# Kernel tuning notes

Measured on AMD Instinct MI355X. Metric: run time of the kernel, lower is better.

## Reference

```python
import jax, jax.numpy as jnp
import numpy as np

B, L, H = 32, 2048, 1024


def setup_inputs() -> dict:
    key = jax.random.key(0)
    k1, k2, k3, k4, k5 = jax.random.split(key, 5)
    stdv = 1.0 / np.sqrt(H)
    return {
        "hidden": jax.random.normal(k1, (B, H), dtype=jnp.float32),
        "encoder_outputs": jax.random.normal(k2, (L, B, H), dtype=jnp.float32),
        "attn_w": jax.random.normal(k3, (H, 2 * H), dtype=jnp.float32) * stdv,
        "attn_b": jax.random.normal(k4, (H,), dtype=jnp.float32) * stdv,
        "v": jax.random.normal(k5, (H,), dtype=jnp.float32) * stdv,
    }


def reference(hidden, encoder_outputs, attn_w, attn_b, v):
    # encoder_outputs: [L, B, H] -> batch-first [B, L, H]
    enc = jnp.transpose(encoder_outputs, (1, 0, 2))
    # Additive (Bahdanau) energies. Split the concat-linear into two GEMMs to
    # avoid materializing the [B, L, 2H] concat:
    #   attn([H_rep, enc]) = hidden @ W_h^T + enc @ W_e^T + b
    w_h, w_e = attn_w[:, :H], attn_w[:, H:]  # each [H, 2H]->[H, H]
    proj = (jnp.einsum("bh,oh->bo", hidden, w_h)[:, None, :]
            + jnp.einsum("blh,oh->blo", enc, w_e)
            + attn_b)
    energy = jnp.tanh(proj)                   # [B, L, H]
    scores = jnp.einsum("blh,h->bl", energy, v)  # [B, L]
    attn = jax.nn.softmax(scores, axis=-1)       # [B, L]
    context = jnp.einsum("bl,blh->bh", attn, enc)  # [B, H]
    return context[None, :, :]  # [1, B, H] matching context.transpose(0,1)
```

## Files before the change

### kernel.cpp

```cpp
#include <hip/hip_runtime.h>
#include <hip/hip_bf16.h>
#include <math.h>

#define Hdim 1024
#define Bdim 32
#define Ldim 2048
#define Mtot (Bdim*Ldim)

typedef __attribute__((ext_vector_type(8))) short short8v;
typedef __attribute__((ext_vector_type(4))) short short4v;
typedef __attribute__((ext_vector_type(4))) float floatx4;

static __device__ inline short f2bf(float f) {
    union { float f; unsigned u; } x; x.f = f;
    unsigned r = x.u + 0x7FFF + ((x.u >> 16) & 1);
    return (short)(r >> 16);
}
static __device__ inline float bf2f(short s) {
    union { unsigned u; float f; } x; x.u = ((unsigned)(unsigned short)s) << 16;
    return x.f;
}

static __device__ inline float fast_tanh(float x) {
    float t = 2.0f * x;
    t = fminf(fmaxf(t, -30.0f), 30.0f);
    float e = __expf(t);
    return (e - 1.0f) / (e + 1.0f);
}

typedef __attribute__((address_space(1))) const void GVT;
typedef __attribute__((address_space(3))) void LVT;
static __device__ inline void gload_lds16(const void* g, void* l) {
    __builtin_amdgcn_global_load_lds((GVT*)g, (LVT*)l, 16, 0, 0);
}

__global__ __launch_bounds__(256) void convert_enc_kernel(
    const float* __restrict__ enc, short* __restrict__ enc_bf)
{
    size_t i = ((size_t)blockIdx.x * 256 + threadIdx.x) * 8;
    float4 a = *(const float4*)(enc + i);
    float4 b = *(const float4*)(enc + i + 4);
    short8v o;
    o[0]=f2bf(a.x); o[1]=f2bf(a.y); o[2]=f2bf(a.z); o[3]=f2bf(a.w);
    o[4]=f2bf(b.x); o[5]=f2bf(b.y); o[6]=f2bf(b.z); o[7]=f2bf(b.w);
    *(short8v*)(enc_bf + i) = o;
}

__global__ __launch_bounds__(256) void convert_w_kernel(
    const float* __restrict__ attn_w, short* __restrict__ w_bf)
{
    int t = blockIdx.x * 256 + threadIdx.x;
    int o = t >> 7;
    int c = t & 127;
    const float* src = attn_w + (size_t)o * 2 * Hdim + Hdim + c * 8;
    float4 a = *(const float4*)(src);
    float4 b = *(const float4*)(src + 4);
    short8v v;
    v[0]=f2bf(a.x); v[1]=f2bf(a.y); v[2]=f2bf(a.z); v[3]=f2bf(a.w);
    v[4]=f2bf(b.x); v[5]=f2bf(b.y); v[6]=f2bf(b.z); v[7]=f2bf(b.w);
    *(short8v*)(w_bf + (size_t)o * Hdim + c * 8) = v;
}

__global__ __launch_bounds__(256) void qproj_kernel(
    const float* __restrict__ hidden, const float* __restrict__ attn_w,
    const float* __restrict__ attn_b, float* __restrict__ qbuf)
{
    int w = blockIdx.x * 4 + (threadIdx.x >> 6);
    int lane = threadIdx.x & 63;
    int o = w >> 5;
    int b = w & 31;
    const float* hrow = hidden + b * Hdim;
    const float* wrow = attn_w + (size_t)o * 2 * Hdim;
    float s = 0.f;
    #pragma unroll
    for (int i = 0; i < 16; i++) s += hrow[lane + i*64] * wrow[lane + i*64];
    s += __shfl_xor(s, 1);  s += __shfl_xor(s, 2);  s += __shfl_xor(s, 4);
    s += __shfl_xor(s, 8);  s += __shfl_xor(s, 16); s += __shfl_xor(s, 32);
    if (lane == 0) qbuf[b * Hdim + o] = s + attn_b[o];
}

#define BM 128
#define BN 128
#define BK 32

__global__ __launch_bounds__(256, 4) void scores_kernel(
    const short* __restrict__ enc_bf,
    const short* __restrict__ w_bf,
    const float* __restrict__ qbuf,
    const float* __restrict__ vvec,
    float* __restrict__ spart)
{
    __shared__ short As[2][BM * BK];
    __shared__ short Bs[2][BN * BK];
    __shared__ float sred[BM][2];

    int hw = blockIdx.x;
    int xcd = hw & 7;
    int i5  = hw >> 3;
    int nblk  = i5 & 7;
    int mtile = xcd * 64 + (i5 >> 3);
    int m0 = mtile * BM;
    int n0 = nblk * BN;

    int tid  = threadIdx.x;
    int w    = tid >> 6;
    int l    = tid & 63;
    int wr = w >> 1, wc = w & 1;
    int r15 = l & 15;
    int kc  = l >> 4;

    int subrow = l >> 2;
    int chunk  = l & 3;
    const short* ag0 = enc_bf + (size_t)(m0 + w*32 + subrow) * Hdim + chunk * 8;
    const short* ag1 = ag0 + (size_t)16 * Hdim;
    const short* bg0 = w_bf  + (size_t)(n0 + w*32 + subrow) * Hdim + chunk * 8;
    const short* bg1 = bg0 + (size_t)16 * Hdim;
    int al0 = (w*32) * BK;
    int al1 = (w*32 + 16) * BK;

    int aoff[4], boff[4];
    #pragma unroll
    for (int i = 0; i < 4; i++) {
        aoff[i] = (wr*64 + i*16 + r15) * BK + kc * 8;
        boff[i] = (wc*64 + i*16 + r15) * BK + kc * 8;
    }

    floatx4 acc[4][4];
    #pragma unroll
    for (int i = 0; i < 4; i++)
        #pragma unroll
        for (int j = 0; j < 4; j++) acc[i][j] = (floatx4){0.f, 0.f, 0.f, 0.f};

    gload_lds16(ag0, &As[0][al0]);
    gload_lds16(ag1, &As[0][al1]);
    gload_lds16(bg0, &Bs[0][al0]);
    gload_lds16(bg1, &Bs[0][al1]);
    ag0 += BK; ag1 += BK; bg0 += BK; bg1 += BK;
    __syncthreads();

    #pragma unroll 2
    for (int kt = 0; kt < Hdim / BK; kt++) {
        int cur = kt & 1;
        if (kt < Hdim / BK - 1) {
            int nxt = cur ^ 1;
            gload_lds16(ag0, &As[nxt][al0]);
            gload_lds16(ag1, &As[nxt][al1]);
            gload_lds16(bg0, &Bs[nxt][al0]);
            gload_lds16(bg1, &Bs[nxt][al1]);
            ag0 += BK; ag1 += BK; bg0 += BK; bg1 += BK;
        }
        short8v af[4], bf[4];
        #pragma unroll
        for (int mi = 0; mi < 4; mi++) af[mi] = *(const short8v*)(&As[cur][aoff[mi]]);
        #pragma unroll
        for (int ni = 0; ni < 4; ni++) bf[ni] = *(const short8v*)(&Bs[cur][boff[ni]]);
        #pragma unroll
        for (int mi = 0; mi < 4; mi++)
            #pragma unroll
            for (int ni = 0; ni < 4; ni++)
                acc[mi][ni] = __builtin_amdgcn_mfma_f32_16x16x32_bf16(af[mi], bf[ni], acc[mi][ni], 0, 0, 0);
        __syncthreads();
    }

    int rg = l >> 4;
    #pragma unroll
    for (int mi = 0; mi < 4; mi++) {
        float rs[4] = {0.f, 0.f, 0.f, 0.f};
        #pragma unroll
        for (int ni = 0; ni < 4; ni++) {
            int o = n0 + wc*64 + ni*16 + r15;
            float vo = vvec[o];
            #pragma unroll
            for (int reg = 0; reg < 4; reg++) {
                int trow = wr*64 + mi*16 + rg*4 + reg;
                int b = trow & 31;
                float p = acc[mi][ni][reg] + qbuf[b * Hdim + o];
                rs[reg] += fast_tanh(p) * vo;
            }
        }
        #pragma unroll
        for (int reg = 0; reg < 4; reg++) {
            float s = rs[reg];
            s += __shfl_xor(s, 1); s += __shfl_xor(s, 2);
            s += __shfl_xor(s, 4); s += __shfl_xor(s, 8);
            if (r15 == 0) {
                int trow = wr*64 + mi*16 + rg*4 + reg;
                sred[trow][wc] = s;
            }
        }
    }
    __syncthreads();
    if (tid < BM)
        spart[(size_t)nblk * Mtot + m0 + tid] = sred[tid][0] + sred[tid][1];
}

__global__ __launch_bounds__(256) void softmax_kernel(
    const float* __restrict__ spart, float* __restrict__ attn)
{
    int b = blockIdx.x;
    int t = threadIdx.x;
    __shared__ float rmax[4], rsum[4];
    float sv[8];
    float mx = -1e30f;
    #pragma unroll
    for (int i = 0; i < 8; i++) {
        int l = t + i * 256;
        int m = l * Bdim + b;
        float s = 0.f;
        #pragma unroll
        for (int p = 0; p < 8; p++) s += spart[(size_t)p * Mtot + m];
        sv[i] = s;
        mx = fmaxf(mx, s);
    }
    #pragma unroll
    for (int off = 1; off < 64; off <<= 1) mx = fmaxf(mx, __shfl_xor(mx, off));
    if ((t & 63) == 0) rmax[t >> 6] = mx;
    __syncthreads();
    mx = fmaxf(fmaxf(rmax[0], rmax[1]), fmaxf(rmax[2], rmax[3]));
    float sum = 0.f;
    #pragma unroll
    for (int i = 0; i < 8; i++) { sv[i] = __expf(sv[i] - mx); sum += sv[i]; }
    #pragma unroll
    for (int off = 1; off < 64; off <<= 1) sum += __shfl_xor(sum, off);
    if ((t & 63) == 0) rsum[t >> 6] = sum;
    __syncthreads();
    sum = rsum[0] + rsum[1] + rsum[2] + rsum[3];
    float inv = 1.f / sum;
    #pragma unroll
    for (int i = 0; i < 8; i++)
        attn[(size_t)b * Ldim + t + i * 256] = sv[i] * inv;
}

__global__ __launch_bounds__(256) void context_part_kernel(
    const short* __restrict__ enc_bf,
    const float* __restrict__ attn,
    float* __restrict__ cpart)
{
    int b = blockIdx.x & 31;
    int c = blockIdx.x >> 5;
    int t = threadIdx.x;
    float a0 = 0.f, a1 = 0.f, a2 = 0.f, a3 = 0.f;
    int l0 = c * 32;
    for (int i = 0; i < 32; i++) {
        int l = l0 + i;
        float a = attn[(size_t)b * Ldim + l];
        short4v e = *(const short4v*)(enc_bf + (size_t)(l * Bdim + b) * Hdim + t * 4);
        a0 += a * bf2f(e.x); a1 += a * bf2f(e.y);
        a2 += a * bf2f(e.z); a3 += a * bf2f(e.w);
    }
    float4 r; r.x = a0; r.y = a1; r.z = a2; r.w = a3;
    *(float4*)(cpart + ((size_t)c * Bdim + b) * Hdim + t * 4) = r;
}

__global__ __launch_bounds__(256) void context_reduce_kernel(
    const float* __restrict__ cpart, float* __restrict__ out)
{
    int idx = blockIdx.x * 256 + threadIdx.x;
    float s = 0.f;
    for (int c = 0; c < 64; c++) s += cpart[(size_t)c * (Bdim * Hdim) + idx];
    out[idx] = s;
}

extern "C" void kernel_launch(void* const* d_in, const int* in_sizes, int n_in,
                              void* d_out, int out_size, void* d_ws, size_t ws_size,
                              hipStream_t stream)
{
    const float* hidden = (const float*)d_in[0];
    const float* enc    = (const float*)d_in[1];
    const float* attn_w = (const float*)d_in[2];
    const float* attn_b = (const float*)d_in[3];
    const float* vvec   = (const float*)d_in[4];
    float* out = (float*)d_out;

    char* ws = (char*)d_ws;
    size_t off = 0;
    short* enc_bf = (short*)(ws + off); off += (size_t)Mtot * Hdim * 2;
    short* w_bf   = (short*)(ws + off); off += (size_t)Hdim * Hdim * 2;
    float* qbuf   = (float*)(ws + off); off += (size_t)Bdim * Hdim * 4;
    float* spart  = (float*)(ws + off); off += (size_t)8 * Mtot * 4;
    float* attnp  = (float*)(ws + off); off += (size_t)Mtot * 4;
    float* cpart  = (float*)(ws + off);

    convert_enc_kernel<<<32768, 256, 0, stream>>>(enc, enc_bf);
    convert_w_kernel<<<512, 256, 0, stream>>>(attn_w, w_bf);
    qproj_kernel<<<8192, 256, 0, stream>>>(hidden, attn_w, attn_b, qbuf);
    scores_kernel<<<4096, 256, 0, stream>>>(enc_bf, w_bf, qbuf, vvec, spart);
    softmax_kernel<<<Bdim, 256, 0, stream>>>(spart, attnp);
    context_part_kernel<<<2048, 256, 0, stream>>>(enc_bf, attnp, cpart);
    context_reduce_kernel<<<128, 256, 0, stream>>>(cpart, out);
}
```

Measured before the change: 306.7 us.

## Fuse encoder bf16 conversion into scores GEMM A-tile load and drop convert pass

Removes the separate kernel that converted the whole encoder tensor to bf16. The scores GEMM now loads fp32 encoder rows into registers, converts them, and writes them into XOR-swizzled LDS, with the conversion of the next tile overlapped with the current MFMA work. The B tile also uses a matching swizzle, and the context kernel now reads fp32 encoder directly. This avoids a full write-then-reread of a 128MB-class intermediate. In exchange, the GEMM reads fp32 A once per N-block (8 times), doubling its A-side bytes, and it uses more registers.

```diff
diff --git a/kernel.cpp b/kernel.cpp
--- a/kernel.cpp
+++ b/kernel.cpp
@@ -16,9 +16,9 @@
     unsigned r = x.u + 0x7FFF + ((x.u >> 16) & 1);
     return (short)(r >> 16);
 }
-static __device__ inline float bf2f(short s) {
-    union { unsigned u; float f; } x; x.u = ((unsigned)(unsigned short)s) << 16;
-    return x.f;
+static __device__ inline short f2bf_hw(float f) {
+    __hip_bfloat16 h = __float2bfloat16(f);
+    return *reinterpret_cast<short*>(&h);
 }
 
 static __device__ inline float fast_tanh(float x) {
@@ -32,18 +32,6 @@
 typedef __attribute__((address_space(3))) void LVT;
 static __device__ inline void gload_lds16(const void* g, void* l) {
     __builtin_amdgcn_global_load_lds((GVT*)g, (LVT*)l, 16, 0, 0);
-}
-
-__global__ __launch_bounds__(256) void convert_enc_kernel(
-    const float* __restrict__ enc, short* __restrict__ enc_bf)
-{
-    size_t i = ((size_t)blockIdx.x * 256 + threadIdx.x) * 8;
-    float4 a = *(const float4*)(enc + i);
-    float4 b = *(const float4*)(enc + i + 4);
-    short8v o;
-    o[0]=f2bf(a.x); o[1]=f2bf(a.y); o[2]=f2bf(a.z); o[3]=f2bf(a.w);
-    o[4]=f2bf(b.x); o[5]=f2bf(b.y); o[6]=f2bf(b.z); o[7]=f2bf(b.w);
-    *(short8v*)(enc_bf + i) = o;
 }
 
 __global__ __launch_bounds__(256) void convert_w_kernel(
@@ -82,9 +70,10 @@
 #define BM 128
 #define BN 128
 #define BK 32
+#define NKT 32
 
 __global__ __launch_bounds__(256, 4) void scores_kernel(
-    const short* __restrict__ enc_bf,
+    const float* __restrict__ enc,
     const short* __restrict__ w_bf,
     const float* __restrict__ qbuf,
     const float* __restrict__ vvec,
@@ -108,22 +97,27 @@
     int wr = w >> 1, wc = w & 1;
     int r15 = l & 15;
     int kc  = l >> 4;
-
-    int subrow = l >> 2;
-    int chunk  = l & 3;
-    const short* ag0 = enc_bf + (size_t)(m0 + w*32 + subrow) * Hdim + chunk * 8;
-    const short* ag1 = ag0 + (size_t)16 * Hdim;
-    const short* bg0 = w_bf  + (size_t)(n0 + w*32 + subrow) * Hdim + chunk * 8;
-    const short* bg1 = bg0 + (size_t)16 * Hdim;
-    int al0 = (w*32) * BK;
-    int al1 = (w*32 + 16) * BK;
-
-    int aoff[4], boff[4];
-    #pragma unroll
-    for (int i = 0; i < 4; i++) {
-        aoff[i] = (wr*64 + i*16 + r15) * BK + kc * 8;
-        boff[i] = (wc*64 + i*16 + r15) * BK + kc * 8;
-    }
+    int rg  = l >> 4;
+
+    int arow = tid >> 2;
+    int acol = tid & 3;
+    int asw  = (tid >> 3) & 3;
+    const float* agp = enc + (size_t)(m0 + arow) * Hdim + acol * 8;
+    const int awoff0 = arow * BK + ((acol ^ asw) * 8);
+    const int awoff1 = (arow + 64) * BK + ((acol ^ asw) * 8);
+
+    const short* bgp = w_bf + (size_t)(n0 + w*32 + (l >> 2)) * Hdim
+                            + (((l & 3) ^ ((l >> 3) & 3)) * 8);
+
+#define STAGE_B(bb, k0) do { \
+    gload_lds16(bgp + (k0),                      &Bs[bb][(w*32)      * BK]); \
+    gload_lds16(bgp + (k0) + 16*(size_t)Hdim,    &Bs[bb][(w*32 + 16) * BK]); \
+} while (0)
+
+    int q = (r15 >> 1) & 3;
+    int rc = (kc ^ q) * 8;
+#define LDA(mi) (*(const short8v*)(&As[cur][(wr*64 + (mi)*16 + r15) * BK + rc]))
+#define LDB(ni) (*(const short8v*)(&Bs[cur][(wc*64 + (ni)*16 + r15) * BK + rc]))
 
     floatx4 acc[4][4];
     #pragma unroll
@@ -131,38 +125,51 @@
         #pragma unroll
         for (int j = 0; j < 4; j++) acc[i][j] = (floatx4){0.f, 0.f, 0.f, 0.f};
 
-    gload_lds16(ag0, &As[0][al0]);
-    gload_lds16(ag1, &As[0][al1]);
-    gload_lds16(bg0, &Bs[0][al0]);
-    gload_lds16(bg1, &Bs[0][al1]);
-    ag0 += BK; ag1 += BK; bg0 += BK; bg1 += BK;
+    float4 a00, a01, a10, a11;
+
+#define LOAD_A(k0) do { \
+    a00 = *(const float4*)(agp + (k0)); \
+    a01 = *(const float4*)(agp + (k0) + 4); \
+    a10 = *(const float4*)(agp + (k0) + 64*(size_t)Hdim); \
+    a11 = *(const float4*)(agp + (k0) + 64*(size_t)Hdim + 4); \
+} while (0)
+#define CVT_WRITE_A(bb) do { \
+    short8v s0, s1; \
+    s0[0]=f2bf_hw(a00.x); s0[1]=f2bf_hw(a00.y); s0[2]=f2bf_hw(a00.z); s0[3]=f2bf_hw(a00.w); \
+    s0[4]=f2bf_hw(a01.x); s0[5]=f2bf_hw(a01.y); s0[6]=f2bf_hw(a01.z); s0[7]=f2bf_hw(a01.w); \
+    s1[0]=f2bf_hw(a10.x); s1[1]=f2bf_hw(a10.y); s1[2]=f2bf_hw(a10.z); s1[3]=f2bf_hw(a10.w); \
+    s1[4]=f2bf_hw(a11.x); s1[5]=f2bf_hw(a11.y); s1[6]=f2bf_hw(a11.z); s1[7]=f2bf_hw(a11.w); \
+    *(short8v*)(&As[bb][awoff0]) = s0; \
+    *(short8v*)(&As[bb][awoff1]) = s1; \
+} while (0)
+
+    LOAD_A(0);
+    STAGE_B(0, 0);
+    CVT_WRITE_A(0);
     __syncthreads();
 
     #pragma unroll 2
-    for (int kt = 0; kt < Hdim / BK; kt++) {
+    for (int kt = 0; kt < NKT; kt++) {
         int cur = kt & 1;
-        if (kt < Hdim / BK - 1) {
-            int nxt = cur ^ 1;
-            gload_lds16(ag0, &As[nxt][al0]);
-            gload_lds16(ag1, &As[nxt][al1]);
-            gload_lds16(bg0, &Bs[nxt][al0]);
-            gload_lds16(bg1, &Bs[nxt][al1]);
-            ag0 += BK; ag1 += BK; bg0 += BK; bg1 += BK;
+        int nxt = cur ^ 1;
+        if (kt < NKT - 1) {
+            LOAD_A((kt + 1) * BK);
+            STAGE_B(nxt, (kt + 1) * BK);
         }
         short8v af[4], bf[4];
         #pragma unroll
-        for (int mi = 0; mi < 4; mi++) af[mi] = *(const short8v*)(&As[cur][aoff[mi]]);
-        #pragma unroll
-        for (int ni = 0; ni < 4; ni++) bf[ni] = *(const short8v*)(&Bs[cur][boff[ni]]);
+        for (int mi = 0; mi < 4; mi++) af[mi] = LDA(mi);
+        #pragma unroll
+        for (int ni = 0; ni < 4; ni++) bf[ni] = LDB(ni);
         #pragma unroll
         for (int mi = 0; mi < 4; mi++)
             #pragma unroll
             for (int ni = 0; ni < 4; ni++)
                 acc[mi][ni] = __builtin_amdgcn_mfma_f32_16x16x32_bf16(af[mi], bf[ni], acc[mi][ni], 0, 0, 0);
+        if (kt < NKT - 1) CVT_WRITE_A(nxt);
         __syncthreads();
     }
 
-    int rg = l >> 4;
     #pragma unroll
     for (int mi = 0; mi < 4; mi++) {
         float rs[4] = {0.f, 0.f, 0.f, 0.f};
@@ -192,10 +199,16 @@
     __syncthreads();
     if (tid < BM)
         spart[(size_t)nblk * Mtot + m0 + tid] = sred[tid][0] + sred[tid][1];
+#undef STAGE_B
+#undef LDA
+#undef LDB
+#undef LOAD_A
+#undef CVT_WRITE_A
 }
 
 __global__ __launch_bounds__(256) void softmax_kernel(
-    const float* __restrict__ spart, float* __restrict__ attn)
+    const float* __restrict__ spart,
+    float* __restrict__ attn)
 {
     int b = blockIdx.x;
     int t = threadIdx.x;
@@ -232,24 +245,22 @@
 }
 
 __global__ __launch_bounds__(256) void context_part_kernel(
-    const short* __restrict__ enc_bf,
+    const float* __restrict__ enc,
     const float* __restrict__ attn,
     float* __restrict__ cpart)
 {
     int b = blockIdx.x & 31;
     int c = blockIdx.x >> 5;
     int t = threadIdx.x;
-    float a0 = 0.f, a1 = 0.f, a2 = 0.f, a3 = 0.f;
+    float4 acc = {0.f, 0.f, 0.f, 0.f};
     int l0 = c * 32;
     for (int i = 0; i < 32; i++) {
         int l = l0 + i;
         float a = attn[(size_t)b * Ldim + l];
-        short4v e = *(const short4v*)(enc_bf + (size_t)(l * Bdim + b) * Hdim + t * 4);
-        a0 += a * bf2f(e.x); a1 += a * bf2f(e.y);
-        a2 += a * bf2f(e.z); a3 += a * bf2f(e.w);
+        float4 e = *(const float4*)(enc + (size_t)(l * Bdim + b) * Hdim + t * 4);
+        acc.x += a * e.x; acc.y += a * e.y; acc.z += a * e.z; acc.w += a * e.w;
     }
-    float4 r; r.x = a0; r.y = a1; r.z = a2; r.w = a3;
-    *(float4*)(cpart + ((size_t)c * Bdim + b) * Hdim + t * 4) = r;
+    *(float4*)(cpart + ((size_t)c * Bdim + b) * Hdim + t * 4) = acc;
 }
 
 __global__ __launch_bounds__(256) void context_reduce_kernel(
@@ -274,18 +285,16 @@
 
     char* ws = (char*)d_ws;
     size_t off = 0;
-    short* enc_bf = (short*)(ws + off); off += (size_t)Mtot * Hdim * 2;
     short* w_bf   = (short*)(ws + off); off += (size_t)Hdim * Hdim * 2;
     float* qbuf   = (float*)(ws + off); off += (size_t)Bdim * Hdim * 4;
     float* spart  = (float*)(ws + off); off += (size_t)8 * Mtot * 4;
     float* attnp  = (float*)(ws + off); off += (size_t)Mtot * 4;
     float* cpart  = (float*)(ws + off);
 
-    convert_enc_kernel<<<32768, 256, 0, stream>>>(enc, enc_bf);
     convert_w_kernel<<<512, 256, 0, stream>>>(attn_w, w_bf);
     qproj_kernel<<<8192, 256, 0, stream>>>(hidden, attn_w, attn_b, qbuf);
-    scores_kernel<<<4096, 256, 0, stream>>>(enc_bf, w_bf, qbuf, vvec, spart);
+    scores_kernel<<<4096, 256, 0, stream>>>(enc, w_bf, qbuf, vvec, spart);
     softmax_kernel<<<Bdim, 256, 0, stream>>>(spart, attnp);
-    context_part_kernel<<<2048, 256, 0, stream>>>(enc_bf, attnp, cpart);
+    context_part_kernel<<<2048, 256, 0, stream>>>(enc, attnp, cpart);
     context_reduce_kernel<<<128, 256, 0, stream>>>(cpart, out);
 }
```

Measured after the change: 293.2 us. -4.4%, faster.

## Switch scores GEMM to 32x32x16 MFMA with XOR-swizzled LDS layout

Applied to the files above, without the earlier changes.

Replaces the 4x4 grid of 16x16x32 bf16 MFMAs per wave with a 2x2 grid of 32x32x16 MFMAs, which covers the same tile with fewer instructions and fewer LDS fragment loads. The global-to-LDS staging now XOR-swizzles 16-byte chunks within each row, and reads apply the same swizzle, to reduce LDS bank conflicts. The fused tanh/v-dot epilogue is reworked for the 32x32 accumulator layout. This risks index-mapping errors in the swizzle or the accumulator row mapping, and the 16-wide accumulators change register pressure.

```diff
diff --git a/kernel.cpp b/kernel.cpp
--- a/kernel.cpp
+++ b/kernel.cpp
@@ -9,7 +9,7 @@
 
 typedef __attribute__((ext_vector_type(8))) short short8v;
 typedef __attribute__((ext_vector_type(4))) short short4v;
-typedef __attribute__((ext_vector_type(4))) float floatx4;
+typedef __attribute__((ext_vector_type(16))) float floatx16;
 
 static __device__ inline short f2bf(float f) {
     union { float f; unsigned u; } x; x.f = f;
@@ -82,6 +82,7 @@
 #define BM 128
 #define BN 128
 #define BK 32
+#define NKT 32
 
 __global__ __launch_bounds__(256, 4) void scores_kernel(
     const short* __restrict__ enc_bf,
@@ -106,96 +107,101 @@
     int w    = tid >> 6;
     int l    = tid & 63;
     int wr = w >> 1, wc = w & 1;
-    int r15 = l & 15;
-    int kc  = l >> 4;
-
-    int subrow = l >> 2;
-    int chunk  = l & 3;
-    const short* ag0 = enc_bf + (size_t)(m0 + w*32 + subrow) * Hdim + chunk * 8;
-    const short* ag1 = ag0 + (size_t)16 * Hdim;
-    const short* bg0 = w_bf  + (size_t)(n0 + w*32 + subrow) * Hdim + chunk * 8;
-    const short* bg1 = bg0 + (size_t)16 * Hdim;
-    int al0 = (w*32) * BK;
-    int al1 = (w*32 + 16) * BK;
-
-    int aoff[4], boff[4];
-    #pragma unroll
-    for (int i = 0; i < 4; i++) {
-        aoff[i] = (wr*64 + i*16 + r15) * BK + kc * 8;
-        boff[i] = (wc*64 + i*16 + r15) * BK + kc * 8;
-    }
-
-    floatx4 acc[4][4];
-    #pragma unroll
-    for (int i = 0; i < 4; i++)
-        #pragma unroll
-        for (int j = 0; j < 4; j++) acc[i][j] = (floatx4){0.f, 0.f, 0.f, 0.f};
-
-    gload_lds16(ag0, &As[0][al0]);
-    gload_lds16(ag1, &As[0][al1]);
-    gload_lds16(bg0, &Bs[0][al0]);
-    gload_lds16(bg1, &Bs[0][al1]);
-    ag0 += BK; ag1 += BK; bg0 += BK; bg1 += BK;
+    int r31 = l & 31;
+    int h   = l >> 5;
+
+    const short* agp = enc_bf + (size_t)(m0 + w*32 + (l >> 2)) * Hdim
+                              + (((l & 3) ^ ((l >> 2) & 3)) * 8);
+    const short* bgp = w_bf  + (size_t)(n0 + w*32 + (l >> 2)) * Hdim
+                              + (((l & 3) ^ ((l >> 2) & 3)) * 8);
+#define STAGE_A(bb, k0) do { \
+    gload_lds16(agp + (k0),                      &As[bb][(w*32)      * BK]); \
+    gload_lds16(agp + (k0) + 16*(size_t)Hdim,    &As[bb][(w*32 + 16) * BK]); \
+} while (0)
+#define STAGE_B(bb, k0) do { \
+    gload_lds16(bgp + (k0),                      &Bs[bb][(w*32)      * BK]); \
+    gload_lds16(bgp + (k0) + 16*(size_t)Hdim,    &Bs[bb][(w*32 + 16) * BK]); \
+} while (0)
+
+    int c0 = ((0*2 + h) ^ (l & 3)) * 8;
+    int c1 = ((1*2 + h) ^ (l & 3)) * 8;
+#define LDA(mi, cc) (*(const short8v*)(&As[cur][(wr*64 + (mi)*32 + r31) * BK + (cc)]))
+#define LDB(ni, cc) (*(const short8v*)(&Bs[cur][(wc*64 + (ni)*32 + r31) * BK + (cc)]))
+
+    floatx16 acc[2][2];
+    #pragma unroll
+    for (int i = 0; i < 2; i++)
+        #pragma unroll
+        for (int j = 0; j < 2; j++)
+            #pragma unroll
+            for (int e = 0; e < 16; e++) acc[i][j][e] = 0.f;
+
+    STAGE_A(0, 0);
+    STAGE_B(0, 0);
     __syncthreads();
 
     #pragma unroll 2
-    for (int kt = 0; kt < Hdim / BK; kt++) {
+    for (int kt = 0; kt < NKT; kt++) {
         int cur = kt & 1;
-        if (kt < Hdim / BK - 1) {
-            int nxt = cur ^ 1;
-            gload_lds16(ag0, &As[nxt][al0]);
-            gload_lds16(ag1, &As[nxt][al1]);
-            gload_lds16(bg0, &Bs[nxt][al0]);
-            gload_lds16(bg1, &Bs[nxt][al1]);
-            ag0 += BK; ag1 += BK; bg0 += BK; bg1 += BK;
+        int nxt = cur ^ 1;
+        if (kt < NKT - 1) {
+            STAGE_A(nxt, (kt + 1) * BK);
+            STAGE_B(nxt, (kt + 1) * BK);
         }
-        short8v af[4], bf[4];
-        #pragma unroll
-        for (int mi = 0; mi < 4; mi++) af[mi] = *(const short8v*)(&As[cur][aoff[mi]]);
-        #pragma unroll
-        for (int ni = 0; ni < 4; ni++) bf[ni] = *(const short8v*)(&Bs[cur][boff[ni]]);
-        #pragma unroll
-        for (int mi = 0; mi < 4; mi++)
+        short8v a0[2], a1[2], b0[2], b1[2];
+        #pragma unroll
+        for (int mi = 0; mi < 2; mi++) { a0[mi] = LDA(mi, c0); a1[mi] = LDA(mi, c1); }
+        #pragma unroll
+        for (int ni = 0; ni < 2; ni++) { b0[ni] = LDB(ni, c0); b1[ni] = LDB(ni, c1); }
+        #pragma unroll
+        for (int mi = 0; mi < 2; mi++)
             #pragma unroll
-            for (int ni = 0; ni < 4; ni++)
-                acc[mi][ni] = __builtin_amdgcn_mfma_f32_16x16x32_bf16(af[mi], bf[ni], acc[mi][ni], 0, 0, 0);
+            for (int ni = 0; ni < 2; ni++) {
+                acc[mi][ni] = __builtin_amdgcn_mfma_f32_32x32x16_bf16(a0[mi], b0[ni], acc[mi][ni], 0, 0, 0);
+                acc[mi][ni] = __builtin_amdgcn_mfma_f32_32x32x16_bf16(a1[mi], b1[ni], acc[mi][ni], 0, 0, 0);
+            }
         __syncthreads();
     }
 
-    int rg = l >> 4;
-    #pragma unroll
-    for (int mi = 0; mi < 4; mi++) {
-        float rs[4] = {0.f, 0.f, 0.f, 0.f};
-        #pragma unroll
-        for (int ni = 0; ni < 4; ni++) {
-            int o = n0 + wc*64 + ni*16 + r15;
+    #pragma unroll
+    for (int mi = 0; mi < 2; mi++) {
+        float rs[16];
+        #pragma unroll
+        for (int reg = 0; reg < 16; reg++) rs[reg] = 0.f;
+        #pragma unroll
+        for (int ni = 0; ni < 2; ni++) {
+            int o = n0 + wc*64 + ni*32 + r31;
             float vo = vvec[o];
             #pragma unroll
-            for (int reg = 0; reg < 4; reg++) {
-                int trow = wr*64 + mi*16 + rg*4 + reg;
-                int b = trow & 31;
-                float p = acc[mi][ni][reg] + qbuf[b * Hdim + o];
+            for (int reg = 0; reg < 16; reg++) {
+                int rloc = (reg & 3) + 8*(reg >> 2) + 4*h;
+                float p = acc[mi][ni][reg] + qbuf[rloc * Hdim + o];
                 rs[reg] += fast_tanh(p) * vo;
             }
         }
         #pragma unroll
-        for (int reg = 0; reg < 4; reg++) {
+        for (int reg = 0; reg < 16; reg++) {
             float s = rs[reg];
-            s += __shfl_xor(s, 1); s += __shfl_xor(s, 2);
-            s += __shfl_xor(s, 4); s += __shfl_xor(s, 8);
-            if (r15 == 0) {
-                int trow = wr*64 + mi*16 + rg*4 + reg;
-                sred[trow][wc] = s;
+            s += __shfl_xor(s, 1); s += __shfl_xor(s, 2); s += __shfl_xor(s, 4);
+            s += __shfl_xor(s, 8); s += __shfl_xor(s, 16);
+            if (r31 == 0) {
+                int r = wr*64 + mi*32 + (reg & 3) + 8*(reg >> 2) + 4*h;
+                sred[r][wc] = s;
             }
         }
     }
     __syncthreads();
     if (tid < BM)
         spart[(size_t)nblk * Mtot + m0 + tid] = sred[tid][0] + sred[tid][1];
+#undef STAGE_A
+#undef STAGE_B
+#undef LDA
+#undef LDB
 }
 
 __global__ __launch_bounds__(256) void softmax_kernel(
-    const float* __restrict__ spart, float* __restrict__ attn)
+    const float* __restrict__ spart,
+    float* __restrict__ attn)
 {
     int b = blockIdx.x;
     int t = threadIdx.x;
```

New measurement: 339.7 us. 10.8% more time.

## Triple-buffer scores GEMM with XOR-swizzled LDS and one barrier per k-step

Applied to the files above, without the earlier changes.

The scores GEMM moves from a double-buffered LDS pipeline with two syncthreads per iteration to a three-stage ring. Each step uses an explicit vmcnt wait and a single s_barrier, and the prefetch is issued two tiles ahead after the fragment reads. The global-to-LDS chunk placement and the fragment reads are XOR-swizzled to avoid LDS bank conflicts, and the MFMA block runs at raised wave priority. This costs more LDS, and the launch-bounds occupancy hint drops from 4 to 3 blocks. It also depends on the vmcnt counting matching the number of outstanding loads.

```diff
diff --git a/kernel.cpp b/kernel.cpp
--- a/kernel.cpp
+++ b/kernel.cpp
@@ -82,16 +82,17 @@
 #define BM 128
 #define BN 128
 #define BK 32
-
-__global__ __launch_bounds__(256, 4) void scores_kernel(
+#define NKT 32
+
+__global__ __launch_bounds__(256, 3) void scores_kernel(
     const short* __restrict__ enc_bf,
     const short* __restrict__ w_bf,
     const float* __restrict__ qbuf,
     const float* __restrict__ vvec,
     float* __restrict__ spart)
 {
-    __shared__ short As[2][BM * BK];
-    __shared__ short Bs[2][BN * BK];
+    __shared__ short As[3][BM * BK];
+    __shared__ short Bs[3][BN * BK];
     __shared__ float sred[BM][2];
 
     int hw = blockIdx.x;
@@ -108,22 +109,25 @@
     int wr = w >> 1, wc = w & 1;
     int r15 = l & 15;
     int kc  = l >> 4;
-
-    int subrow = l >> 2;
-    int chunk  = l & 3;
-    const short* ag0 = enc_bf + (size_t)(m0 + w*32 + subrow) * Hdim + chunk * 8;
-    const short* ag1 = ag0 + (size_t)16 * Hdim;
-    const short* bg0 = w_bf  + (size_t)(n0 + w*32 + subrow) * Hdim + chunk * 8;
-    const short* bg1 = bg0 + (size_t)16 * Hdim;
-    int al0 = (w*32) * BK;
-    int al1 = (w*32 + 16) * BK;
-
-    int aoff[4], boff[4];
-    #pragma unroll
-    for (int i = 0; i < 4; i++) {
-        aoff[i] = (wr*64 + i*16 + r15) * BK + kc * 8;
-        boff[i] = (wc*64 + i*16 + r15) * BK + kc * 8;
-    }
+    int rg  = l >> 4;
+
+    const short* agp = enc_bf + (size_t)(m0 + w*32 + (l >> 2)) * Hdim
+                              + (((l & 3) ^ ((l >> 3) & 3)) * 8);
+    const short* bgp = w_bf  + (size_t)(n0 + w*32 + (l >> 2)) * Hdim
+                              + (((l & 3) ^ ((l >> 3) & 3)) * 8);
+#define STAGE_A(bb, k0) do { \
+    gload_lds16(agp + (k0),                      &As[bb][(w*32)      * BK]); \
+    gload_lds16(agp + (k0) + 16*(size_t)Hdim,    &As[bb][(w*32 + 16) * BK]); \
+} while (0)
+#define STAGE_B(bb, k0) do { \
+    gload_lds16(bgp + (k0),                      &Bs[bb][(w*32)      * BK]); \
+    gload_lds16(bgp + (k0) + 16*(size_t)Hdim,    &Bs[bb][(w*32 + 16) * BK]); \
+} while (0)
+
+    int q2 = (r15 >> 1) & 3;
+    int rc = (kc ^ q2) * 8;
+#define LDA(mi) (*(const short8v*)(&As[cur][(wr*64 + (mi)*16 + r15) * BK + rc]))
+#define LDB(ni) (*(const short8v*)(&Bs[cur][(wc*64 + (ni)*16 + r15) * BK + rc]))
 
     floatx4 acc[4][4];
     #pragma unroll
@@ -131,38 +135,38 @@
         #pragma unroll
         for (int j = 0; j < 4; j++) acc[i][j] = (floatx4){0.f, 0.f, 0.f, 0.f};
 
-    gload_lds16(ag0, &As[0][al0]);
-    gload_lds16(ag1, &As[0][al1]);
-    gload_lds16(bg0, &Bs[0][al0]);
-    gload_lds16(bg1, &Bs[0][al1]);
-    ag0 += BK; ag1 += BK; bg0 += BK; bg1 += BK;
-    __syncthreads();
-
-    #pragma unroll 2
-    for (int kt = 0; kt < Hdim / BK; kt++) {
-        int cur = kt & 1;
-        if (kt < Hdim / BK - 1) {
-            int nxt = cur ^ 1;
-            gload_lds16(ag0, &As[nxt][al0]);
-            gload_lds16(ag1, &As[nxt][al1]);
-            gload_lds16(bg0, &Bs[nxt][al0]);
-            gload_lds16(bg1, &Bs[nxt][al1]);
-            ag0 += BK; ag1 += BK; bg0 += BK; bg1 += BK;
+    STAGE_A(0, 0);      STAGE_B(0, 0);
+    STAGE_A(1, BK);     STAGE_B(1, BK);
+
+    int cur = 0;
+    for (int t = 0; t < NKT; t++) {
+        if (t < NKT - 1) asm volatile("s_waitcnt vmcnt(4)" ::: "memory");
+        else             asm volatile("s_waitcnt vmcnt(0)" ::: "memory");
+        __builtin_amdgcn_s_barrier();
+
+        short8v af[4], bf[4];
+        #pragma unroll
+        for (int mi = 0; mi < 4; mi++) af[mi] = LDA(mi);
+        #pragma unroll
+        for (int ni = 0; ni < 4; ni++) bf[ni] = LDB(ni);
+
+        if (t + 2 < NKT) {
+            int nb = cur + 2; if (nb >= 3) nb -= 3;
+            STAGE_A(nb, (t + 2) * BK);
+            STAGE_B(nb, (t + 2) * BK);
         }
-        short8v af[4], bf[4];
-        #pragma unroll
-        for (int mi = 0; mi < 4; mi++) af[mi] = *(const short8v*)(&As[cur][aoff[mi]]);
-        #pragma unroll
-        for (int ni = 0; ni < 4; ni++) bf[ni] = *(const short8v*)(&Bs[cur][boff[ni]]);
+
+        __builtin_amdgcn_s_setprio(1);
         #pragma unroll
         for (int mi = 0; mi < 4; mi++)
             #pragma unroll
             for (int ni = 0; ni < 4; ni++)
                 acc[mi][ni] = __builtin_amdgcn_mfma_f32_16x16x32_bf16(af[mi], bf[ni], acc[mi][ni], 0, 0, 0);
-        __syncthreads();
+        __builtin_amdgcn_s_setprio(0);
+
+        cur++; if (cur >= 3) cur -= 3;
     }
 
-    int rg = l >> 4;
     #pragma unroll
     for (int mi = 0; mi < 4; mi++) {
         float rs[4] = {0.f, 0.f, 0.f, 0.f};
@@ -192,10 +196,15 @@
     __syncthreads();
     if (tid < BM)
         spart[(size_t)nblk * Mtot + m0 + tid] = sred[tid][0] + sred[tid][1];
+#undef STAGE_A
+#undef STAGE_B
+#undef LDA
+#undef LDB
 }
 
 __global__ __launch_bounds__(256) void softmax_kernel(
-    const float* __restrict__ spart, float* __restrict__ attn)
+    const float* __restrict__ spart,
+    float* __restrict__ attn)
 {
     int b = blockIdx.x;
     int t = threadIdx.x;
```

After: 306.6 us. No clear change (-0.0%).
